# Kernel tuning notes

Hardware: AMD Instinct MI355X
Metric: run time of the kernel (lower is better)

The kernel has to match this reference:

```python
import jax, jax.numpy as jnp
import numpy as np
from jax import lax

M = 4194304      # total ray samples
N_RAYS = 16384   # number of rays
INTERVAL = 0.5
ALPHA_INIT = 1e-6


def setup_inputs() -> dict:
    key = jax.random.key(0)
    k1, k2, k3 = jax.random.split(key, 3)
    density = jax.random.normal(k1, (M,), dtype=jnp.float32)
    rgb_raw = jax.random.normal(k2, (M, 3), dtype=jnp.float32)
    # act_shift buffer: log(1/(1-alpha_init) - 1)
    shift = jnp.full((1,), np.log(1.0 / (1.0 - ALPHA_INIT) - 1.0), dtype=jnp.float32)
    ray_id = jnp.sort(jax.random.randint(k3, (M,), 0, N_RAYS, dtype=jnp.int32))
    return {"density": density, "rgb_raw": rgb_raw, "shift": shift,
            "ray_id": ray_id, "N": N_RAYS}


def _seg_comb(a, b):
    # associative operator for segmented product scan: (prod, reset_flag)
    pa, fa = a
    pb, fb = b
    return jnp.where(fb, pb, pa * pb), fa | fb


def reference(density, rgb_raw, shift, ray_id, N):
    # Raw2Alpha: alpha = 1 - exp(-softplus(density + shift) * interval)
    s = jax.nn.softplus(density + shift[0]) * INTERVAL   # [M], >= 0
    alpha = -jnp.expm1(-s)                                # 1 - exp(-s), stable
    om = jnp.exp(-s)                                      # 1 - alpha, exact

    # Alphas2Weights: per-ray transmittance scan over variable-length segments.
    first = jnp.concatenate([jnp.ones((1,), bool), ray_id[1:] != ray_id[:-1]])
    # inclusive segmented cumprod of (1 - alpha)
    Tin, _ = lax.associative_scan(_seg_comb, (om, first))
    # exclusive transmittance: T_i = prod of (1-alpha_j) for j earlier in same ray
    T = jnp.where(first, 1.0, jnp.concatenate([jnp.ones((1,), om.dtype), Tin[:-1]]))
    weights = alpha * T                                   # [M]
    # leftover transmittance per ray (1 for rays with no samples)
    alphainv_last = jax.ops.segment_prod(om, ray_id, num_segments=N)  # [N]

    # alpha compositing of colors against a white background
    rgb = jax.nn.sigmoid(rgb_raw)                          # [M,3]
    rgb_marched = (jax.ops.segment_sum(weights[:, None] * rgb, ray_id, num_segments=N)
                   + alphainv_last[:, None])               # [N,3]
    return rgb_marched
```

## Files before the change

### kernel.cpp

```cpp
#include <hip/hip_runtime.h>
#include <math.h>


__device__ __forceinline__ float sigm(float x) {
    return __builtin_amdgcn_rcpf(1.0f + __expf(-x));
}

__global__ __launch_bounds__(256) void seg_starts_kernel(
    const int* __restrict__ ray_id, int* __restrict__ starts, int M, int N)
{
    const int i4 = (blockIdx.x * 256 + threadIdx.x) * 4;
    if (i4 >= M) return;

    if (i4 + 3 < M) {
        const int4 v = *(const int4*)(ray_id + i4);
        const int prev = (i4 == 0) ? -1 : ray_id[i4 - 1];
        int c0 = prev, c1 = v.x, c2 = v.y, c3 = v.z, c4 = v.w;
        for (int r = c0 + 1; r <= c1; ++r) starts[r] = i4 + 0;
        for (int r = c1 + 1; r <= c2; ++r) starts[r] = i4 + 1;
        for (int r = c2 + 1; r <= c3; ++r) starts[r] = i4 + 2;
        for (int r = c3 + 1; r <= c4; ++r) starts[r] = i4 + 3;
        if (i4 + 4 == M) {
            for (int r = c4 + 1; r <= N; ++r) starts[r] = M;
        }
    } else {
        int prev = (i4 == 0) ? -1 : ray_id[i4 - 1];
        for (int k = 0; k < 4 && i4 + k < M; ++k) {
            const int cur = ray_id[i4 + k];
            for (int r = prev + 1; r <= cur; ++r) starts[r] = i4 + k;
            prev = cur;
            if (i4 + k == M - 1)
                for (int r = cur + 1; r <= N; ++r) starts[r] = M;
        }
    }
}

__global__ __launch_bounds__(256) void voxel_march_kernel(
    const float* __restrict__ density,
    const float* __restrict__ rgb_raw,
    const float* __restrict__ shift,
    const int*   __restrict__ starts,
    float* __restrict__ out,
    int M, int N)
{
    const int lane = threadIdx.x & 63;
    const int wave = threadIdx.x >> 6;
    const int ray  = blockIdx.x * 4 + wave;
    if (ray >= N) return;

    const float sh = shift[0];
    const int begin = starts[ray];
    const int end   = starts[ray + 1];

    float carry = 1.0f;
    float acc0 = 0.0f, acc1 = 0.0f, acc2 = 0.0f;

    float4 dA, a0A, a1A, a2A;
    float4 dB, a0B, a1B, a2B;

    auto issue = [&](int base, float4& dd, float4& r0, float4& r1, float4& r2) {
        const int b4 = base + 4 * lane;
        const int ba = min(b4, M - 4);
        dd = *(const float4*)(density + ba);
        const float4* rp = (const float4*)(rgb_raw + 3 * ba);
        r0 = rp[0]; r1 = rp[1]; r2 = rp[2];
    };

    auto compute = [&](int base, const float4& dd, const float4& c0,
                       const float4& c1, const float4& c2) {
        const int b4 = base + 4 * lane;
        const bool v0 = (b4 + 0 >= begin) & (b4 + 0 < end);
        const bool v1 = (b4 + 1 >= begin) & (b4 + 1 < end);
        const bool v2 = (b4 + 2 >= begin) & (b4 + 2 < end);
        const bool v3 = (b4 + 3 >= begin) & (b4 + 3 < end);
        const float d0 = v0 ? dd.x : -1e30f;
        const float d1 = v1 ? dd.y : -1e30f;
        const float d2 = v2 ? dd.z : -1e30f;
        const float d3 = v3 ? dd.w : -1e30f;

        const float om0 = __builtin_amdgcn_rsqf(1.0f + __expf(d0 + sh));
        const float om1 = __builtin_amdgcn_rsqf(1.0f + __expf(d1 + sh));
        const float om2 = __builtin_amdgcn_rsqf(1.0f + __expf(d2 + sh));
        const float om3 = __builtin_amdgcn_rsqf(1.0f + __expf(d3 + sh));
        const float al0 = 1.0f - om0, al1 = 1.0f - om1;
        const float al2 = 1.0f - om2, al3 = 1.0f - om3;

        float p = (om0 * om1) * (om2 * om3);
        #pragma unroll
        for (int off = 1; off < 64; off <<= 1) {
            float q = __shfl_up(p, off, 64);
            if (lane >= off) p *= q;
        }
        float excl = __shfl_up(p, 1, 64);
        if (lane == 0) excl = 1.0f;

        float t = carry * excl;
        const float w0 = al0 * t; t *= om0;
        const float w1 = al1 * t; t *= om1;
        const float w2 = al2 * t; t *= om2;
        const float w3 = al3 * t;

        acc0 += w0 * sigm(c0.x) + w1 * sigm(c0.w) + w2 * sigm(c1.z) + w3 * sigm(c2.y);
        acc1 += w0 * sigm(c0.y) + w1 * sigm(c1.x) + w2 * sigm(c1.w) + w3 * sigm(c2.z);
        acc2 += w0 * sigm(c0.z) + w1 * sigm(c1.y) + w2 * sigm(c2.x) + w3 * sigm(c2.w);

        carry *= __shfl(p, 63, 64);
    };

    int base = begin & ~3;
    if (base < end) {
        issue(base, dA, a0A, a1A, a2A);
        while (true) {
            int nb = base + 256;
            const bool moreB = nb < end;
            if (moreB) issue(nb, dB, a0B, a1B, a2B);
            compute(base, dA, a0A, a1A, a2A);
            if (!moreB) break;
            base = nb;
            nb = base + 256;
            const bool moreA = nb < end;
            if (moreA) issue(nb, dA, a0A, a1A, a2A);
            compute(base, dB, a0B, a1B, a2B);
            if (!moreA) break;
            base = nb;
        }
    }

    #pragma unroll
    for (int off = 32; off > 0; off >>= 1) {
        acc0 += __shfl_down(acc0, off, 64);
        acc1 += __shfl_down(acc1, off, 64);
        acc2 += __shfl_down(acc2, off, 64);
    }

    if (lane == 0) {
        out[3 * ray + 0] = acc0 + carry;
        out[3 * ray + 1] = acc1 + carry;
        out[3 * ray + 2] = acc2 + carry;
    }
}

extern "C" void kernel_launch(void* const* d_in, const int* in_sizes, int n_in,
                              void* d_out, int out_size, void* d_ws, size_t ws_size,
                              hipStream_t stream)
{
    const float* density = (const float*)d_in[0];
    const float* rgb_raw = (const float*)d_in[1];
    const float* shift   = (const float*)d_in[2];
    const int*   ray_id  = (const int*)d_in[3];
    float* out = (float*)d_out;

    const int M = in_sizes[0];
    const int N = out_size / 3;

    int* starts = (int*)d_ws;
    const int t1 = (M + 3) / 4;
    seg_starts_kernel<<<(t1 + 255) / 256, 256, 0, stream>>>(ray_id, starts, M, N);

    const int rays_per_block = 4;
    const int blocks = (N + rays_per_block - 1) / rays_per_block;
    voxel_march_kernel<<<blocks, 256, 0, stream>>>(density, rgb_raw, shift,
                                                   starts, out, M, N);
}
```

Baseline: 113.3 us.

## Process eight samples per lane per chunk and drop explicit double buffering

Each lane now handles 8 consecutive samples per iteration (512 per wave chunk) instead of 4, with wider loads of density and rgb. The manual A/B double-buffered prefetch is removed in favour of a simple loop. With about 256 samples per ray, most rays now fit in a single chunk, which halves the shuffle-scan passes and amortises overhead. The cost is more wasted lanes at segment edges and the loss of explicit load/compute overlap.

After: 114.7 us. About the same (+1.2%).

```diff
diff --git a/kernel.cpp b/kernel.cpp
--- a/kernel.cpp
+++ b/kernel.cpp
@@ -15,13 +15,12 @@
     if (i4 + 3 < M) {
         const int4 v = *(const int4*)(ray_id + i4);
         const int prev = (i4 == 0) ? -1 : ray_id[i4 - 1];
-        int c0 = prev, c1 = v.x, c2 = v.y, c3 = v.z, c4 = v.w;
-        for (int r = c0 + 1; r <= c1; ++r) starts[r] = i4 + 0;
-        for (int r = c1 + 1; r <= c2; ++r) starts[r] = i4 + 1;
-        for (int r = c2 + 1; r <= c3; ++r) starts[r] = i4 + 2;
-        for (int r = c3 + 1; r <= c4; ++r) starts[r] = i4 + 3;
+        for (int r = prev + 1; r <= v.x; ++r) starts[r] = i4 + 0;
+        for (int r = v.x + 1; r <= v.y; ++r) starts[r] = i4 + 1;
+        for (int r = v.y + 1; r <= v.z; ++r) starts[r] = i4 + 2;
+        for (int r = v.z + 1; r <= v.w; ++r) starts[r] = i4 + 3;
         if (i4 + 4 == M) {
-            for (int r = c4 + 1; r <= N; ++r) starts[r] = M;
+            for (int r = v.w + 1; r <= N; ++r) starts[r] = M;
         }
     } else {
         int prev = (i4 == 0) ? -1 : ray_id[i4 - 1];
@@ -55,37 +54,37 @@
     float carry = 1.0f;
     float acc0 = 0.0f, acc1 = 0.0f, acc2 = 0.0f;
 
-    float4 dA, a0A, a1A, a2A;
-    float4 dB, a0B, a1B, a2B;
+    for (int base = (begin & ~7); base < end; base += 512) {
+        const int b8 = base + 8 * lane;
+        const int ba = min(b8, M - 8);
 
-    auto issue = [&](int base, float4& dd, float4& r0, float4& r1, float4& r2) {
-        const int b4 = base + 4 * lane;
-        const int ba = min(b4, M - 4);
-        dd = *(const float4*)(density + ba);
+        const float4 dd0 = *(const float4*)(density + ba);
+        const float4 dd1 = *(const float4*)(density + ba + 4);
         const float4* rp = (const float4*)(rgb_raw + 3 * ba);
-        r0 = rp[0]; r1 = rp[1]; r2 = rp[2];
-    };
+        float r[24];
+        {
+            const float4 q0 = rp[0], q1 = rp[1], q2 = rp[2];
+            const float4 q3 = rp[3], q4 = rp[4], q5 = rp[5];
+            r[0]=q0.x;  r[1]=q0.y;  r[2]=q0.z;  r[3]=q0.w;
+            r[4]=q1.x;  r[5]=q1.y;  r[6]=q1.z;  r[7]=q1.w;
+            r[8]=q2.x;  r[9]=q2.y;  r[10]=q2.z; r[11]=q2.w;
+            r[12]=q3.x; r[13]=q3.y; r[14]=q3.z; r[15]=q3.w;
+            r[16]=q4.x; r[17]=q4.y; r[18]=q4.z; r[19]=q4.w;
+            r[20]=q5.x; r[21]=q5.y; r[22]=q5.z; r[23]=q5.w;
+        }
+        float d[8] = {dd0.x, dd0.y, dd0.z, dd0.w, dd1.x, dd1.y, dd1.z, dd1.w};
 
-    auto compute = [&](int base, const float4& dd, const float4& c0,
-                       const float4& c1, const float4& c2) {
-        const int b4 = base + 4 * lane;
-        const bool v0 = (b4 + 0 >= begin) & (b4 + 0 < end);
-        const bool v1 = (b4 + 1 >= begin) & (b4 + 1 < end);
-        const bool v2 = (b4 + 2 >= begin) & (b4 + 2 < end);
-        const bool v3 = (b4 + 3 >= begin) & (b4 + 3 < end);
-        const float d0 = v0 ? dd.x : -1e30f;
-        const float d1 = v1 ? dd.y : -1e30f;
-        const float d2 = v2 ? dd.z : -1e30f;
-        const float d3 = v3 ? dd.w : -1e30f;
+        float om[8], al[8];
+        #pragma unroll
+        for (int k = 0; k < 8; ++k) {
+            const int j = b8 + k;
+            const bool v = (j >= begin) & (j < end);
+            const float x = (v ? d[k] : -1e30f) + sh;
+            om[k] = __builtin_amdgcn_rsqf(1.0f + __expf(x));
+            al[k] = 1.0f - om[k];
+        }
 
-        const float om0 = __builtin_amdgcn_rsqf(1.0f + __expf(d0 + sh));
-        const float om1 = __builtin_amdgcn_rsqf(1.0f + __expf(d1 + sh));
-        const float om2 = __builtin_amdgcn_rsqf(1.0f + __expf(d2 + sh));
-        const float om3 = __builtin_amdgcn_rsqf(1.0f + __expf(d3 + sh));
-        const float al0 = 1.0f - om0, al1 = 1.0f - om1;
-        const float al2 = 1.0f - om2, al3 = 1.0f - om3;
-
-        float p = (om0 * om1) * (om2 * om3);
+        float p = ((om[0]*om[1])*(om[2]*om[3])) * ((om[4]*om[5])*(om[6]*om[7]));
         #pragma unroll
         for (int off = 1; off < 64; off <<= 1) {
             float q = __shfl_up(p, off, 64);
@@ -95,35 +94,16 @@
         if (lane == 0) excl = 1.0f;
 
         float t = carry * excl;
-        const float w0 = al0 * t; t *= om0;
-        const float w1 = al1 * t; t *= om1;
-        const float w2 = al2 * t; t *= om2;
-        const float w3 = al3 * t;
-
-        acc0 += w0 * sigm(c0.x) + w1 * sigm(c0.w) + w2 * sigm(c1.z) + w3 * sigm(c2.y);
-        acc1 += w0 * sigm(c0.y) + w1 * sigm(c1.x) + w2 * sigm(c1.w) + w3 * sigm(c2.z);
-        acc2 += w0 * sigm(c0.z) + w1 * sigm(c1.y) + w2 * sigm(c2.x) + w3 * sigm(c2.w);
+        #pragma unroll
+        for (int k = 0; k < 8; ++k) {
+            const float w = al[k] * t;
+            acc0 += w * sigm(r[3*k+0]);
+            acc1 += w * sigm(r[3*k+1]);
+            acc2 += w * sigm(r[3*k+2]);
+            t *= om[k];
+        }
 
         carry *= __shfl(p, 63, 64);
-    };
-
-    int base = begin & ~3;
-    if (base < end) {
-        issue(base, dA, a0A, a1A, a2A);
-        while (true) {
-            int nb = base + 256;
-            const bool moreB = nb < end;
-            if (moreB) issue(nb, dB, a0B, a1B, a2B);
-            compute(base, dA, a0A, a1A, a2A);
-            if (!moreB) break;
-            base = nb;
-            nb = base + 256;
-            const bool moreA = nb < end;
-            if (moreA) issue(nb, dA, a0A, a1A, a2A);
-            compute(base, dB, a0B, a1B, a2B);
-            if (!moreA) break;
-            base = nb;
-        }
     }
 
     #pragma unroll
```
